# Kernel optimization log

Hardware: AMD Instinct MI355X
Metric: run time of the kernel (lower is better)

## Reference

```python
import jax, jax.numpy as jnp
import numpy as np
from jax import lax
from jax.scipy.special import logsumexp

N = 1024   # keypoints image 0
M = 1024   # keypoints image 1
D = 256    # descriptor dim
H = 4      # attention heads
L = 18     # GNN layers ('self','cross')*9
ITERS = 100
KENC = [4, 32, 64, 128, 256]


def conv1(x, w, b):
    # 1x1 Conv1d == channel matmul: x [b,c,n], w [o,c], b [o]
    return jnp.einsum('oc,bcn->bon', w, x) + b[None, :, None]


def inorm(x, eps=1e-5):
    # InstanceNorm1d (affine=False): normalize over length per (b, c)
    m = jnp.mean(x, axis=-1, keepdims=True)
    v = jnp.var(x, axis=-1, keepdims=True)
    return (x - m) * lax.rsqrt(v + eps)


def attention_block(x, src, pw, pb, mw, mb):
    b, d, _ = x.shape
    dh = d // H
    q = conv1(x, pw[0], pb[0]).reshape(b, dh, H, -1)
    k = conv1(src, pw[1], pb[1]).reshape(b, dh, H, -1)
    v = conv1(src, pw[2], pb[2]).reshape(b, dh, H, -1)
    s = jnp.einsum('bdhn,bdhm->bhnm', q, k) / (dh ** 0.5)
    p = jax.nn.softmax(s, axis=-1)
    o = jnp.einsum('bhnm,bdhm->bdhn', p, v).reshape(b, d, -1)
    return conv1(o, mw, mb)


def prop(x, src, i, Pw, Pb, Mw, Mb, W0, B0, W1, B1):
    msg = attention_block(x, src, Pw[i], Pb[i], Mw[i], Mb[i])
    h = jnp.concatenate([x, msg], axis=1)          # [b, 2D, n]
    h = jax.nn.relu(inorm(conv1(h, W0[i], B0[i])))
    return conv1(h, W1[i], B1[i])


def sinkhorn(Z, log_mu, log_nu, iters):
    def step(carry, _):
        u, v = carry
        u = log_mu - logsumexp(Z + v[:, None, :], axis=2)
        v = log_nu - logsumexp(Z + u[:, :, None], axis=1)
        return (u, v), None
    init = (jnp.zeros_like(log_mu), jnp.zeros_like(log_nu))
    (u, v), _ = lax.scan(jax.checkpoint(step), init, None, length=iters)
    return Z + u[:, :, None] + v[:, None, :]


def log_optimal_transport(scores, alpha, iters):
    b, m, n = scores.shape
    bins0 = jnp.broadcast_to(alpha, (b, m, 1))
    bins1 = jnp.broadcast_to(alpha, (b, 1, n))
    binsA = jnp.broadcast_to(alpha, (b, 1, 1))
    couplings = jnp.concatenate([
        jnp.concatenate([scores, bins0], axis=-1),
        jnp.concatenate([bins1, binsA], axis=-1)], axis=1)  # [b, m+1, n+1]
    norm = np.float32(-np.log(m + n))
    log_mu = jnp.concatenate([jnp.full((m,), norm, scores.dtype),
                              jnp.array([np.log(n)], scores.dtype) + norm])
    log_nu = jnp.concatenate([jnp.full((n,), norm, scores.dtype),
                              jnp.array([np.log(m)], scores.dtype) + norm])
    log_mu = jnp.broadcast_to(log_mu[None], (b, m + 1))
    log_nu = jnp.broadcast_to(log_nu[None], (b, n + 1))
    Z = sinkhorn(couplings, log_mu, log_nu, iters)
    return Z - norm


def setup_inputs() -> dict:
    key = jax.random.key(0)
    ks = iter(jax.random.split(key, 64))
    w = lambda shape, s=0.02: jax.random.normal(next(ks), shape, jnp.float32) * s
    inp = {
        'keypoints0': jax.random.normal(next(ks), (1, N, 3), jnp.float32),
        'keypoints1': jax.random.normal(next(ks), (1, M, 3), jnp.float32),
        'descriptors0': jax.random.normal(next(ks), (1, D, N), jnp.float32),
        'descriptors1': jax.random.normal(next(ks), (1, D, M), jnp.float32),
        'scores0': jax.random.uniform(next(ks), (1, N), jnp.float32),
        'scores1': jax.random.uniform(next(ks), (1, M), jnp.float32),
    }
    for i in range(4):
        inp[f'kenc_w{i}'] = w((KENC[i + 1], KENC[i]), 0.1)
        inp[f'kenc_b{i}'] = jnp.zeros((KENC[i + 1],), jnp.float32)
    inp['gnn_proj_w'] = w((L, 3, D, D))
    inp['gnn_proj_b'] = jnp.zeros((L, 3, D), jnp.float32)
    inp['gnn_merge_w'] = w((L, D, D))
    inp['gnn_merge_b'] = jnp.zeros((L, D), jnp.float32)
    inp['gnn_mlp_w0'] = w((L, 2 * D, 2 * D))
    inp['gnn_mlp_b0'] = jnp.zeros((L, 2 * D), jnp.float32)
    inp['gnn_mlp_w1'] = w((L, D, 2 * D))
    inp['gnn_mlp_b1'] = jnp.zeros((L, D), jnp.float32)
    inp['final_w'] = w((D, D))
    inp['final_b'] = jnp.zeros((D,), jnp.float32)
    inp['bin_score'] = jnp.float32(1.0)
    return inp


def reference(keypoints0, keypoints1, descriptors0, descriptors1, scores0, scores1,
              kenc_w0, kenc_b0, kenc_w1, kenc_b1, kenc_w2, kenc_b2, kenc_w3, kenc_b3,
              gnn_proj_w, gnn_proj_b, gnn_merge_w, gnn_merge_b,
              gnn_mlp_w0, gnn_mlp_b0, gnn_mlp_w1, gnn_mlp_b1,
              final_w, final_b, bin_score):
    def kenc(kpts, sc):
        h = jnp.concatenate([jnp.swapaxes(kpts, 1, 2), sc[:, None, :]], axis=1)  # [b,4,n]
        h = jax.nn.relu(inorm(conv1(h, kenc_w0, kenc_b0)))
        h = jax.nn.relu(inorm(conv1(h, kenc_w1, kenc_b1)))
        h = jax.nn.relu(inorm(conv1(h, kenc_w2, kenc_b2)))
        return conv1(h, kenc_w3, kenc_b3)

    d0 = descriptors0 + kenc(keypoints0, scores0)
    d1 = descriptors1 + kenc(keypoints1, scores1)
    for i in range(L):  # even: self, odd: cross
        cross = (i % 2 == 1)
        s0 = d1 if cross else d0
        s1 = d0 if cross else d1
        delta0 = prop(d0, s0, i, gnn_proj_w, gnn_proj_b, gnn_merge_w, gnn_merge_b,
                      gnn_mlp_w0, gnn_mlp_b0, gnn_mlp_w1, gnn_mlp_b1)
        delta1 = prop(d1, s1, i, gnn_proj_w, gnn_proj_b, gnn_merge_w, gnn_merge_b,
                      gnn_mlp_w0, gnn_mlp_b0, gnn_mlp_w1, gnn_mlp_b1)
        d0, d1 = d0 + delta0, d1 + delta1
    md0 = conv1(d0, final_w, final_b)
    md1 = conv1(d1, final_w, final_b)
    scores = jnp.einsum('bdn,bdm->bnm', md0, md1) / (D ** 0.5)
    return log_optimal_transport(scores, bin_score, ITERS)
```

## Files before the change

### kernel.cpp

```cpp
#include <hip/hip_runtime.h>
#include <cstddef>

#define TPB 256

typedef _Float16 f16;
typedef _Float16 f16x4 __attribute__((ext_vector_type(4)));
typedef _Float16 f16x8 __attribute__((ext_vector_type(8)));
typedef float f32x4 __attribute__((ext_vector_type(4)));

__device__ __forceinline__ float block_sum(float v, float* red) {
  int tid = threadIdx.x;
  red[tid] = v; __syncthreads();
#pragma unroll
  for (int off = 128; off > 0; off >>= 1) {
    if (tid < off) red[tid] += red[tid + off];
    __syncthreads();
  }
  float r = red[0];
  __syncthreads();
  return r;
}

__global__ __launch_bounds__(TPB) void build_h0(const float* __restrict__ kp0,
                                                const float* __restrict__ kp1,
                                                const float* __restrict__ sc0,
                                                const float* __restrict__ sc1,
                                                float* __restrict__ h0) {
  int n = blockIdx.x * TPB + threadIdx.x;
  int im = blockIdx.y;
  const float* kp = im ? kp1 : kp0;
  const float* sc = im ? sc1 : sc0;
  float* h = h0 + (size_t)im * 4096;
  h[n]        = kp[n * 3 + 0];
  h[1024 + n] = kp[n * 3 + 1];
  h[2048 + n] = kp[n * 3 + 2];
  h[3072 + n] = sc[n];
}

template<bool NORMRELU, bool RESID>
__global__ __launch_bounds__(TPB) void chanconv(const float* __restrict__ W,
                                                const float* __restrict__ bias,
                                                const float* __restrict__ in, long instride,
                                                const float* res0, const float* res1,
                                                float* __restrict__ out, long outstride, int C) {
  int o = blockIdx.x, im = blockIdx.y, tid = threadIdx.x;
  const float* inp = in + (long)im * instride;
  __shared__ float Ws[128];
  __shared__ float red[TPB];
  for (int c = tid; c < C; c += TPB) Ws[c] = W[(long)o * C + c];
  __syncthreads();
  float b = bias[o];
  float4 acc = {b, b, b, b};
  for (int c = 0; c < C; ++c) {
    float w = Ws[c];
    float4 v = *(const float4*)(inp + (long)c * 1024 + tid * 4);
    acc.x += w * v.x; acc.y += w * v.y; acc.z += w * v.z; acc.w += w * v.w;
  }
  float* orow = out + (long)im * outstride + (long)o * 1024;
  if (NORMRELU) {
    float s = acc.x + acc.y + acc.z + acc.w;
    float mean = block_sum(s, red) * (1.f / 1024.f);
    float dx = acc.x - mean, dy = acc.y - mean, dz = acc.z - mean, dw = acc.w - mean;
    float var = block_sum(dx * dx + dy * dy + dz * dz + dw * dw, red) * (1.f / 1024.f);
    float rstd = rsqrtf(var + 1e-5f);
    float4 o4 = {fmaxf(dx * rstd, 0.f), fmaxf(dy * rstd, 0.f),
                 fmaxf(dz * rstd, 0.f), fmaxf(dw * rstd, 0.f)};
    *(float4*)(orow + tid * 4) = o4;
  } else {
    if (RESID) {
      const float* res = im ? res1 : res0;
      float4 r = *(const float4*)(res + (long)o * 1024 + tid * 4);
      acc.x += r.x; acc.y += r.y; acc.z += r.z; acc.w += r.w;
    }
    *(float4*)(orow + tid * 4) = acc;
  }
}

struct GBH {
  const void* A; const void* B; const void* B2; void* C;
  const float* bias; const float* res; const float* mu; const float* rs;
  void* o2a; void* o2b; int coff; int pad;
};
struct GB16 { GBH g[16]; };

#define F_BNORM   1
#define F_BCONCAT 2
#define F_BADD    4
#define F_CD16    8
#define F_RES     16
#define F_OUT2    32
#define F_CSCAT   64

template<int BN, int ASRC, int BSRC, int FLAGS>
__global__ __launch_bounds__(TPB) void gemmh(GB16 gbs, int K, int lda, int ldb,
                                             int ldc, float alpha, int ksplit) {
  constexpr int WN = BN / 2;
  constexpr int NFR = WN / 16;
  GBH g = gbs.g[blockIdx.z];
  const int tid = threadIdx.x;
  const int lane = tid & 63, wid = tid >> 6;
  const int wm = wid >> 1, wn = wid & 1;
  const int m0 = blockIdx.y * 64, n0 = blockIdx.x * BN;
  __shared__ f16 As[64][36];
  __shared__ f16 Bs[BN][36];
  f32x4 acc[2][NFR];
#pragma unroll
  for (int i = 0; i < 2; ++i)
#pragma unroll
    for (int j = 0; j < NFR; ++j) acc[i][j] = (f32x4){0.f, 0.f, 0.f, 0.f};

  for (int k0 = 0; k0 < K; k0 += 32) {
    if constexpr (ASRC == 0) {
      const int m = tid >> 2, k4 = (tid & 3) * 8;
      const float* ap = (const float*)g.A + (long)(m0 + m) * lda + k0 + k4;
      float4 u0 = *(const float4*)ap, u1 = *(const float4*)(ap + 4);
      f16x4 h0 = {(f16)u0.x, (f16)u0.y, (f16)u0.z, (f16)u0.w};
      f16x4 h1 = {(f16)u1.x, (f16)u1.y, (f16)u1.z, (f16)u1.w};
      *(f16x4*)&As[m][k4] = h0;
      *(f16x4*)&As[m][k4 + 4] = h1;
    } else if constexpr (ASRC == 1) {
      const int k = tid >> 3, mg = (tid & 7) * 8;
      const f16* ap = (const f16*)g.A + (long)(k0 + k) * lda + m0 + mg;
      f16x8 h = *(const f16x8*)ap;
#pragma unroll
      for (int j = 0; j < 8; ++j) As[mg + j][k] = h[j];
    } else {
      const int m = tid >> 2, k4 = (tid & 3) * 8;
      const f16* ap = (const f16*)g.A + (long)(m0 + m) * lda + k0 + k4;
      f16x8 h = *(const f16x8*)ap;
      const float M = g.mu[m0 + m], Iv = g.rs[m0 + m];
      f16x4 h0, h1;
#pragma unroll
      for (int j = 0; j < 4; ++j) h0[j] = (f16)(__expf((float)h[j] - M) * Iv);
#pragma unroll
      for (int j = 0; j < 4; ++j) h1[j] = (f16)(__expf((float)h[j + 4] - M) * Iv);
      *(f16x4*)&As[m][k4] = h0;
      *(f16x4*)&As[m][k4 + 4] = h1;
    }
#pragma unroll
    for (int r = 0; r < BN / 64; ++r) {
      if constexpr (BSRC == 0) {
        const int k = tid >> 3, ng = (tid & 7) * 8 + r * 64;
        const int kg = k0 + k;
        const float* bp;
        if constexpr ((FLAGS & F_BCONCAT) != 0)
          bp = (kg < ksplit) ? ((const float*)g.B + (long)kg * ldb)
                             : ((const float*)g.B2 + (long)(kg - ksplit) * ldb);
        else
          bp = (const float*)g.B + (long)kg * ldb;
        float4 u0 = *(const float4*)(bp + n0 + ng);
        float4 u1 = *(const float4*)(bp + n0 + ng + 4);
        Bs[ng + 0][k] = (f16)u0.x; Bs[ng + 1][k] = (f16)u0.y;
        Bs[ng + 2][k] = (f16)u0.z; Bs[ng + 3][k] = (f16)u0.w;
        Bs[ng + 4][k] = (f16)u1.x; Bs[ng + 5][k] = (f16)u1.y;
        Bs[ng + 6][k] = (f16)u1.z; Bs[ng + 7][k] = (f16)u1.w;
      } else if constexpr (BSRC == 1) {
        const int k = tid >> 3, ng = (tid & 7) * 8 + r * 64;
        const int kg = k0 + k;
        f16x8 h = *(const f16x8*)((const f16*)g.B + (long)kg * ldb + n0 + ng);
        if constexpr ((FLAGS & F_BNORM) != 0) {
          const float mu = g.mu[kg], rs = g.rs[kg];
#pragma unroll
          for (int j = 0; j < 8; ++j)
            h[j] = (f16)fmaxf(((float)h[j] - mu) * rs, 0.f);
        }
#pragma unroll
        for (int j = 0; j < 8; ++j) Bs[ng + j][k] = h[j];
      } else {
        const int n = (tid >> 2) + r * 64, k4 = (tid & 3) * 8;
        const f16* bp = (const f16*)g.B + (long)(n0 + n) * ldb + k0 + k4;
        f16x8 h = *(const f16x8*)bp;
        if constexpr ((FLAGS & F_BADD) != 0) {
          f16x8 h2 = *(const f16x8*)((const f16*)g.B2 + (long)(n0 + n) * ldb + k0 + k4);
          h = h + h2;
        }
        f16x4 h0 = {h[0], h[1], h[2], h[3]};
        f16x4 h1 = {h[4], h[5], h[6], h[7]};
        *(f16x4*)&Bs[n][k4] = h0;
        *(f16x4*)&Bs[n][k4 + 4] = h1;
      }
    }
    __syncthreads();
#pragma unroll
    for (int ks = 0; ks < 2; ++ks) {
      const int kof = ks * 16 + ((lane >> 4) << 2);
      f16x4 a[2], b[NFR];
      a[0] = *(const f16x4*)&As[wm * 32 + (lane & 15)][kof];
      a[1] = *(const f16x4*)&As[wm * 32 + 16 + (lane & 15)][kof];
#pragma unroll
      for (int fn = 0; fn < NFR; ++fn)
        b[fn] = *(const f16x4*)&Bs[wn * WN + fn * 16 + (lane & 15)][kof];
#pragma unroll
      for (int fm = 0; fm < 2; ++fm)
#pragma unroll
        for (int fn = 0; fn < NFR; ++fn)
          acc[fm][fn] = __builtin_amdgcn_mfma_f32_16x16x16f16(a[fm], b[fn], acc[fm][fn], 0, 0, 0);
    }
    __syncthreads();
  }

  const int r0 = (lane >> 4) << 2, cn = lane & 15;
#pragma unroll
  for (int fm = 0; fm < 2; ++fm) {
#pragma unroll
    for (int r = 0; r < 4; ++r) {
      const int m = m0 + wm * 32 + fm * 16 + r0 + r;
      const float bi = g.bias ? g.bias[m] : 0.f;
#pragma unroll
      for (int fn = 0; fn < NFR; ++fn) {
        const int n = n0 + wn * WN + fn * 16 + cn;
        float v = acc[fm][fn][r] * alpha + bi;
        if constexpr ((FLAGS & F_RES) != 0) v += g.res[(long)m * ldc + n];
        if constexpr ((FLAGS & F_OUT2) != 0) {
          ((float*)g.C)[(long)m * 1028 + n] = v;
          ((f16*)g.o2a)[(long)m * 1028 + n] = (f16)v;
          ((f16*)g.o2b)[(long)n * 1028 + m] = (f16)v;
        } else if constexpr ((FLAGS & F_CSCAT) != 0) {
          ((f16*)g.C)[(long)m * ldc + g.coff + 4 * n] = (f16)v;
        } else if constexpr ((FLAGS & F_CD16) != 0) {
          ((f16*)g.C)[(long)m * ldc + n] = (f16)v;
        } else {
          ((float*)g.C)[(long)m * ldc + n] = v;
        }
      }
    }
  }
}

__global__ __launch_bounds__(TPB) void rowlse_h(const f16* __restrict__ S,
                                                float* __restrict__ Mrow,
                                                float* __restrict__ Inv) {
  int row = blockIdx.x * 4 + (threadIdx.x >> 6);
  int lane = threadIdx.x & 63;
  const f16x8* p = (const f16x8*)(S + (long)row * 1024);
  f16x8 v0 = p[lane], v1 = p[lane + 64];
  float m = -1e30f;
#pragma unroll
  for (int j = 0; j < 8; ++j)
    m = fmaxf(m, fmaxf((float)v0[j], (float)v1[j]));
#pragma unroll
  for (int off = 32; off > 0; off >>= 1) m = fmaxf(m, __shfl_xor(m, off));
  float s = 0.f;
#pragma unroll
  for (int j = 0; j < 8; ++j)
    s += __expf((float)v0[j] - m) + __expf((float)v1[j] - m);
#pragma unroll
  for (int off = 32; off > 0; off >>= 1) s += __shfl_xor(s, off);
  if (lane == 0) { Mrow[row] = m; Inv[row] = 1.f / s; }
}

__global__ __launch_bounds__(TPB) void rowstats2_h(const f16* __restrict__ t,
                                                   float* __restrict__ mu,
                                                   float* __restrict__ rs) {
  int row = blockIdx.x * 4 + (threadIdx.x >> 6);
  int lane = threadIdx.x & 63;
  const f16x8* p = (const f16x8*)(t + (long)row * 1024);
  f16x8 v0 = p[lane], v1 = p[lane + 64];
  float s = 0.f, s2 = 0.f;
#pragma unroll
  for (int j = 0; j < 8; ++j) {
    float a = (float)v0[j], b = (float)v1[j];
    s += a + b; s2 += a * a + b * b;
  }
#pragma unroll
  for (int off = 32; off > 0; off >>= 1) { s += __shfl_xor(s, off); s2 += __shfl_xor(s2, off); }
  if (lane == 0) {
    float mean = s * (1.f / 1024.f);
    mu[row] = mean;
    rs[row] = rsqrtf(fmaxf(s2 * (1.f / 1024.f) - mean * mean, 0.f) + 1e-5f);
  }
}

#define NORMC  (-7.62461899f)
#define LOGN   (6.93147181f)
#define LOG_MN (7.62461899f)
#define ZLD    1028

__global__ __launch_bounds__(TPB) void fill_bins(float* __restrict__ Z,
                                                 f16* __restrict__ Zh,
                                                 f16* __restrict__ Zth,
                                                 const float* __restrict__ alpha_p) {
  float a = *alpha_p;
  int t = blockIdx.x * TPB + threadIdx.x;
  if (t <= 1024) {
    Z[(long)t * ZLD + 1024] = a;
    Z[(long)1024 * ZLD + t] = a;
    Zh[(long)t * ZLD + 1024] = (f16)a;
    Zh[(long)1024 * ZLD + t] = (f16)a;
    Zth[(long)t * ZLD + 1024] = (f16)a;
    Zth[(long)1024 * ZLD + t] = (f16)a;
#pragma unroll
    for (int j = 0; j < 3; ++j) {
      Zh[(long)t * ZLD + 1025 + j] = (f16)(-1e30f);
      Zth[(long)t * ZLD + 1025 + j] = (f16)(-1e30f);
    }
  }
}

__global__ __launch_bounds__(TPB) void vinit(float* __restrict__ v) {
  int t = blockIdx.x * TPB + threadIdx.x;
  if (t < ZLD) v[t] = 0.f;
}

__global__ __launch_bounds__(TPB) void sink2h(const f16* __restrict__ Zm,
                                              const float* __restrict__ w,
                                              float* __restrict__ out) {
  int row = blockIdx.x * 4 + (threadIdx.x >> 6);
  if (row > 1024) return;
  int lane = threadIdx.x & 63;
  const f16x4* zp = (const f16x4*)(Zm + (long)row * ZLD);
  const float4* wp = (const float4*)w;
  float m = -1e30f, s = 0.f;
#pragma unroll
  for (int c = 0; c < 5; ++c) {
    int idx = lane + 64 * c;
    if (idx < 257) {
      f16x4 z = zp[idx];
      float4 wv = wp[idx];
      float v0 = (float)z[0] + wv.x, v1 = (float)z[1] + wv.y;
      float v2 = (float)z[2] + wv.z, v3 = (float)z[3] + wv.w;
      float m4 = fmaxf(fmaxf(v0, v1), fmaxf(v2, v3));
      float mn = fmaxf(m, m4);
      s = s * __expf(m - mn) + __expf(v0 - mn) + __expf(v1 - mn)
        + __expf(v2 - mn) + __expf(v3 - mn);
      m = mn;
    }
  }
#pragma unroll
  for (int off = 32; off > 0; off >>= 1) {
    float mo = __shfl_xor(m, off), so = __shfl_xor(s, off);
    float mn = fmaxf(m, mo);
    s = s * __expf(m - mn) + so * __expf(mo - mn);
    m = mn;
  }
  if (lane == 0) {
    float mu = (row < 1024) ? NORMC : (NORMC + LOGN);
    out[row] = mu - (m + logf(s));
  }
}

__global__ __launch_bounds__(TPB) void assemble(const float* __restrict__ Z,
                                                const float* __restrict__ u,
                                                const float* __restrict__ v,
                                                float* __restrict__ out) {
  int idx = blockIdx.x * TPB + threadIdx.x;
  if (idx < 1025 * 1025) {
    int i = idx / 1025;
    int j = idx - i * 1025;
    out[idx] = Z[(long)i * ZLD + j] + u[i] + v[j] + LOG_MN;
  }
}

static inline GBH mkgb(const void* A, const void* B, void* C,
                       const float* bias = nullptr, const void* B2 = nullptr,
                       const float* res = nullptr,
                       const float* mu = nullptr, const float* rs = nullptr,
                       int coff = 0, void* o2a = nullptr, void* o2b = nullptr) {
  GBH g; g.A = A; g.B = B; g.B2 = B2; g.C = C; g.bias = bias; g.res = res;
  g.mu = mu; g.rs = rs; g.o2a = o2a; g.o2b = o2b; g.coff = coff; g.pad = 0;
  return g;
}

extern "C" void kernel_launch(void* const* d_in, const int* in_sizes, int n_in,
                              void* d_out, int out_size, void* d_ws, size_t ws_size,
                              hipStream_t stream) {
  const float* kp0     = (const float*)d_in[0];
  const float* kp1     = (const float*)d_in[1];
  const float* desc0   = (const float*)d_in[2];
  const float* desc1   = (const float*)d_in[3];
  const float* sc0     = (const float*)d_in[4];
  const float* sc1     = (const float*)d_in[5];
  const float* kw[4]   = {(const float*)d_in[6], (const float*)d_in[8],
                          (const float*)d_in[10], (const float*)d_in[12]};
  const float* kb[4]   = {(const float*)d_in[7], (const float*)d_in[9],
                          (const float*)d_in[11], (const float*)d_in[13]};
  const float* proj_w  = (const float*)d_in[14];
  const float* proj_b  = (const float*)d_in[15];
  const float* merge_w = (const float*)d_in[16];
  const float* merge_b = (const float*)d_in[17];
  const float* mlp_w0  = (const float*)d_in[18];
  const float* mlp_b0  = (const float*)d_in[19];
  const float* mlp_w1  = (const float*)d_in[20];
  const float* mlp_b1  = (const float*)d_in[21];
  const float* final_w = (const float*)d_in[22];
  const float* final_b = (const float*)d_in[23];
  const float* alpha_p = (const float*)d_in[24];

  float* p = (float*)d_ws;
  float* dA  = p; p += 524288;
  float* dB  = p; p += 524288;
  float* h0  = p; p += 8192;
  float* hb1 = p; p += 262144;
  float* hb2 = p; p += 131072;
  float* msg = p; p += 524288;
  float* muA = p; p += 1024;
  float* rsA = p; p += 1024;
  float* Mrw = p; p += 8192;
  float* Inv = p; p += 8192;
  float* Zb  = p; p += 1053700;
  float* ub  = p; p += 1028;
  float* vb  = p; p += 1028;
  f16* qkvh = (f16*)p; p += 786432;
  f16* Sh   = (f16*)p; p += 4194304;
  f16* oAh  = (f16*)p; p += 262144;
  f16* oBh  = (f16*)p; p += 262144;
  f16* tbh  = (f16*)p; p += 524288;
  f16* mdbh = (f16*)p; p += 262144;
  f16* Zh   = (f16*)p; p += 526852;
  f16* Zth  = (f16*)p; p += 526852;
  size_t need_bytes = (size_t)(p - (float*)d_ws) * sizeof(float);
  if (ws_size < need_bytes) return;

  const long DSTR = 262144;

  build_h0<<<dim3(4, 2), TPB, 0, stream>>>(kp0, kp1, sc0, sc1, h0);
  chanconv<true, false><<<dim3(32, 2),  TPB, 0, stream>>>(kw[0], kb[0], h0,  4096,   nullptr, nullptr, hb1, 32768,  4);
  chanconv<true, false><<<dim3(64, 2),  TPB, 0, stream>>>(kw[1], kb[1], hb1, 32768,  nullptr, nullptr, hb2, 65536,  32);
  chanconv<true, false><<<dim3(128, 2), TPB, 0, stream>>>(kw[2], kb[2], hb2, 65536,  nullptr, nullptr, hb1, 131072, 64);
  chanconv<false, true><<<dim3(256, 2), TPB, 0, stream>>>(kw[3], kb[3], hb1, 131072, desc0,   desc1,   dA,  DSTR,   128);

  float* dc = dA;
  float* dn = dB;
  for (int i = 0; i < 18; ++i) {
    bool cross = (i & 1) != 0;
    const float* xs[2] = {dc, dc + DSTR};
    const float* ss2[2] = {cross ? xs[1] : xs[0], cross ? xs[0] : xs[1]};

    {
      GB16 gb{};
      for (int im = 0; im < 2; ++im)
        for (int pp = 0; pp < 3; ++pp)
          gb.g[im * 3 + pp] = mkgb(proj_w + (size_t)(i * 3 + pp) * 65536,
                                   (pp == 0 ? xs[im] : ss2[im]),
                                   qkvh + (size_t)(im * 3 + pp) * DSTR,
                                   proj_b + (size_t)(i * 3 + pp) * 256);
      gemmh<128, 0, 0, F_CD16><<<dim3(8, 4, 6), TPB, 0, stream>>>(
          gb, 256, 256, 1024, 1024, 1.f, 0);
    }
    {
      GB16 gb{};
      for (int im = 0; im < 2; ++im)
        for (int h = 0; h < 4; ++h)
          gb.g[im * 4 + h] = mkgb(qkvh + (size_t)(im * 3 + 0) * DSTR + h * 1024,
                                  qkvh + (size_t)(im * 3 + 1) * DSTR + h * 1024,
                                  Sh + (size_t)(im * 4 + h) * 1048576);
      gemmh<128, 1, 1, F_CD16><<<dim3(8, 16, 8), TPB, 0, stream>>>(
          gb, 64, 4096, 4096, 1024, 0.125f, 0);
    }
    rowlse_h<<<2048, TPB, 0, stream>>>(Sh, Mrw, Inv);
    {
      GB16 gb{};
      for (int kh = 0; kh < 2; ++kh)
        for (int imh = 0; imh < 8; ++imh) {
          int im = imh >> 2, h = imh & 3;
          gb.g[kh * 8 + imh] = mkgb(Sh + (size_t)imh * 1048576 + kh * 512,
                                    qkvh + (size_t)(im * 3 + 2) * DSTR + h * 1024 + kh * 512,
                                    (kh ? oBh : oAh) + (size_t)im * 262144,
                                    nullptr, nullptr, nullptr,
                                    Mrw + imh * 1024, Inv + imh * 1024, h);
        }
      gemmh<64, 2, 2, F_CD16 | F_CSCAT><<<dim3(1, 16, 16), TPB, 0, stream>>>(
          gb, 512, 1024, 4096, 256, 1.f, 0);
    }
    {
      GB16 gb{};
      for (int im = 0; im < 2; ++im)
        gb.g[im] = mkgb(merge_w + (size_t)i * 65536, oAh + (size_t)im * 262144,
                        msg + (size_t)im * DSTR, merge_b + (size_t)i * 256,
                        oBh + (size_t)im * 262144);
      gemmh<64, 0, 2, F_BADD><<<dim3(16, 4, 2), TPB, 0, stream>>>(
          gb, 256, 256, 256, 1024, 1.f, 0);
    }
    {
      GB16 gb{};
      for (int im = 0; im < 2; ++im)
        gb.g[im] = mkgb(mlp_w0 + (size_t)i * 262144, xs[im],
                        tbh + (size_t)im * 524288, mlp_b0 + (size_t)i * 512,
                        msg + (size_t)im * DSTR);
      gemmh<64, 0, 0, F_BCONCAT | F_CD16><<<dim3(16, 8, 2), TPB, 0, stream>>>(
          gb, 512, 512, 1024, 1024, 1.f, 256);
    }
    rowstats2_h<<<256, TPB, 0, stream>>>(tbh, muA, rsA);
    {
      GB16 gb{};
      for (int im = 0; im < 2; ++im)
        gb.g[im] = mkgb(mlp_w1 + (size_t)i * 131072, tbh + (size_t)im * 524288,
                        dn + (size_t)im * DSTR, mlp_b1 + (size_t)i * 256,
                        nullptr, xs[im],
                        muA + (size_t)im * 512, rsA + (size_t)im * 512);
      gemmh<64, 0, 1, F_BNORM | F_RES><<<dim3(16, 4, 2), TPB, 0, stream>>>(
          gb, 512, 512, 1024, 1024, 1.f, 0);
    }
    float* tmp = dc; dc = dn; dn = tmp;
  }

  {
    GB16 gb{};
    for (int im = 0; im < 2; ++im)
      gb.g[im] = mkgb(final_w, dc + (size_t)im * DSTR, mdbh + (size_t)im * 262144,
                      final_b);
    gemmh<64, 0, 0, F_CD16><<<dim3(16, 4, 2), TPB, 0, stream>>>(
        gb, 256, 256, 1024, 1024, 1.f, 0);
  }
  {
    GB16 gb{};
    gb.g[0] = mkgb(mdbh, mdbh + 262144, Zb, nullptr, nullptr, nullptr,
                   nullptr, nullptr, 0, Zh, Zth);
    gemmh<64, 1, 1, F_OUT2><<<dim3(16, 16, 1), TPB, 0, stream>>>(
        gb, 256, 1024, 1024, ZLD, 0.0625f, 0);
  }
  fill_bins<<<5, TPB, 0, stream>>>(Zb, Zh, Zth, alpha_p);
  vinit<<<5, TPB, 0, stream>>>(vb);

  for (int it = 0; it < 100; ++it) {
    sink2h<<<257, TPB, 0, stream>>>(Zh, vb, ub);
    sink2h<<<257, TPB, 0, stream>>>(Zth, ub, vb);
  }

  assemble<<<4105, TPB, 0, stream>>>(Zb, ub, vb, (float*)d_out);
}
```

Measured before the change: 2.120 ms.

## Fuse Sinkhorn iterations into one persistent kernel with a software grid barrier

The 200 per-iteration Sinkhorn launches become a single persistent kernel of 128 blocks. Each wave handles two rows, plus the bin row for wave zero, and the u and v half-steps are separated by an atomic-counter grid barrier. Vector init and barrier reset move into fill_bins, which removes the vinit launch. This cuts launch overhead and trades 257-block parallelism for fewer blocks, and it relies on all 128 blocks being co-resident, otherwise the barrier can deadlock.

```diff
diff --git a/kernel.cpp b/kernel.cpp
--- a/kernel.cpp
+++ b/kernel.cpp
@@ -275,13 +275,18 @@
 #define LOGN   (6.93147181f)
 #define LOG_MN (7.62461899f)
 #define ZLD    1028
+#define SINKB  128
 
 __global__ __launch_bounds__(TPB) void fill_bins(float* __restrict__ Z,
                                                  f16* __restrict__ Zh,
                                                  f16* __restrict__ Zth,
-                                                 const float* __restrict__ alpha_p) {
+                                                 const float* __restrict__ alpha_p,
+                                                 float* __restrict__ vb,
+                                                 unsigned* __restrict__ bar) {
   float a = *alpha_p;
   int t = blockIdx.x * TPB + threadIdx.x;
+  if (t < ZLD) vb[t] = 0.f;
+  if (t == 0) *bar = 0u;
   if (t <= 1024) {
     Z[(long)t * ZLD + 1024] = a;
     Z[(long)1024 * ZLD + t] = a;
@@ -297,17 +302,10 @@
   }
 }
 
-__global__ __launch_bounds__(TPB) void vinit(float* __restrict__ v) {
-  int t = blockIdx.x * TPB + threadIdx.x;
-  if (t < ZLD) v[t] = 0.f;
-}
-
-__global__ __launch_bounds__(TPB) void sink2h(const f16* __restrict__ Zm,
-                                              const float* __restrict__ w,
-                                              float* __restrict__ out) {
-  int row = blockIdx.x * 4 + (threadIdx.x >> 6);
-  if (row > 1024) return;
-  int lane = threadIdx.x & 63;
+__device__ __forceinline__ void sink_row(const f16* __restrict__ Zm,
+                                         const float* __restrict__ w,
+                                         float* __restrict__ out,
+                                         int row, int lane) {
   const f16x4* zp = (const f16x4*)(Zm + (long)row * ZLD);
   const float4* wp = (const float4*)w;
   float m = -1e30f, s = 0.f;
@@ -336,6 +334,39 @@
   if (lane == 0) {
     float mu = (row < 1024) ? NORMC : (NORMC + LOGN);
     out[row] = mu - (m + logf(s));
+  }
+}
+
+__device__ __forceinline__ void gridbar(unsigned* __restrict__ bar, unsigned gen) {
+  __syncthreads();
+  if (threadIdx.x == 0) {
+    __threadfence();
+    __hip_atomic_fetch_add(bar, 1u, __ATOMIC_ACQ_REL, __HIP_MEMORY_SCOPE_AGENT);
+    const unsigned target = gen * SINKB;
+    while (__hip_atomic_load(bar, __ATOMIC_ACQUIRE, __HIP_MEMORY_SCOPE_AGENT) < target)
+      __builtin_amdgcn_s_sleep(1);
+  }
+  __syncthreads();
+}
+
+__global__ __launch_bounds__(TPB) void sink_persist(const f16* __restrict__ Zh,
+                                                    const f16* __restrict__ Zth,
+                                                    float* __restrict__ ub,
+                                                    float* __restrict__ vb,
+                                                    unsigned* __restrict__ bar) {
+  const int lane = threadIdx.x & 63;
+  const int gw = blockIdx.x * 4 + (threadIdx.x >> 6);
+  unsigned gen = 0;
+#pragma unroll 1
+  for (int it = 0; it < 100; ++it) {
+    sink_row(Zh, vb, ub, gw, lane);
+    sink_row(Zh, vb, ub, gw + 512, lane);
+    if (gw == 0) sink_row(Zh, vb, ub, 1024, lane);
+    gridbar(bar, ++gen);
+    sink_row(Zth, ub, vb, gw, lane);
+    sink_row(Zth, ub, vb, gw + 512, lane);
+    if (gw == 0) sink_row(Zth, ub, vb, 1024, lane);
+    gridbar(bar, ++gen);
   }
 }
 
@@ -400,6 +431,7 @@
   float* Zb  = p; p += 1053700;
   float* ub  = p; p += 1028;
   float* vb  = p; p += 1028;
+  unsigned* bar = (unsigned*)p; p += 4;
   f16* qkvh = (f16*)p; p += 786432;
   f16* Sh   = (f16*)p; p += 4194304;
   f16* oAh  = (f16*)p; p += 262144;
@@ -509,13 +541,9 @@
     gemmh<64, 1, 1, F_OUT2><<<dim3(16, 16, 1), TPB, 0, stream>>>(
         gb, 256, 1024, 1024, ZLD, 0.0625f, 0);
   }
-  fill_bins<<<5, TPB, 0, stream>>>(Zb, Zh, Zth, alpha_p);
-  vinit<<<5, TPB, 0, stream>>>(vb);
-
-  for (int it = 0; it < 100; ++it) {
-    sink2h<<<257, TPB, 0, stream>>>(Zh, vb, ub);
-    sink2h<<<257, TPB, 0, stream>>>(Zth, ub, vb);
-  }
+  fill_bins<<<5, TPB, 0, stream>>>(Zb, Zh, Zth, alpha_p, vb, bar);
+
+  sink_persist<<<SINKB, TPB, 0, stream>>>(Zh, Zth, ub, vb, bar);
 
   assemble<<<4105, TPB, 0, stream>>>(Zb, ub, vb, (float*)d_out);
 }
```

Result: slower. 3.220 ms (+51.9%).
